# Optimization experiments

Hardware: AMD Instinct MI355X
Metric: run time of the kernel (lower is better)

## Reference

```python
import jax, jax.numpy as jnp
import numpy as np
import math

ANSWER_LEN = 11; D_MODEL = 6; FFN_DIM = 3; HEAD_DIM = 3; MAX_SEQ_LEN = 34
N_HEADS = 2; POS_DIM = 3; TOK_DIM = 3; VOCAB_SIZE = 14; MAX_DIGITS = 10
EOS_TOKEN = 12; EQUALS_TOKEN = 11; PAD_TOKEN = 13; PLUS_TOKEN = 10
B, T = 65536, 34


def _spiral(i, period):
    return (math.cos(2 * math.pi * i / period), math.sin(2 * math.pi * i / period), i / max(period - 1, 1))


def _build_pos_enc():
    N_POS = 10
    pe = np.zeros((MAX_SEQ_LEN, POS_DIM), dtype=np.float32)
    for i in range(MAX_DIGITS):
        pe[i] = _spiral(i, N_POS)
    for i in range(MAX_DIGITS):
        pe[11 + i] = _spiral(i, N_POS)
    for i in range(min(ANSWER_LEN, N_POS)):
        pe[22 + i] = _spiral(i, N_POS)
    pe[32] = [0.0, 0.0, 1.5]
    pe[10] = [2.0, 0.0, -1.0]
    pe[21] = [0.0, 2.0, -1.0]
    pe[33] = [-2.0, 0.0, -1.0]
    return pe


def _build_tok_emb():
    emb = np.zeros((VOCAB_SIZE, TOK_DIM), dtype=np.float32)
    for d in range(10):
        emb[d] = _spiral(d, 10)
    emb[PLUS_TOKEN] = [2.0, 0.0, -1.0]
    emb[EQUALS_TOKEN] = [0.0, 2.0, -1.0]
    emb[EOS_TOKEN] = [-2.0, 0.0, -1.0]
    emb[PAD_TOKEN] = [0.0, -2.0, -1.0]
    return emb


def setup_inputs() -> dict:
    key = jax.random.key(0)
    ks = jax.random.split(key, 12)
    H = N_HEADS * HEAD_DIM  # 6

    def lin(k, out_d, in_d):
        bound = 1.0 / math.sqrt(in_d)
        return jax.random.uniform(k, (out_d, in_d), jnp.float32, -bound, bound)

    return {
        'idx': jax.random.randint(ks[0], (B, T), 0, VOCAB_SIZE),
        'tok_emb': jnp.asarray(_build_tok_emb()),
        'pos_enc': jnp.asarray(_build_pos_enc()),
        'q_w': lin(ks[1], H, POS_DIM),
        'k_w': lin(ks[2], H, POS_DIM),
        'v_w': lin(ks[3], H, TOK_DIM),
        'out_w': lin(ks[4], D_MODEL, H),
        'ln1_g': jnp.ones((D_MODEL,)), 'ln1_b': jnp.zeros((D_MODEL,)),
        'ln2_g': jnp.ones((D_MODEL,)), 'ln2_b': jnp.zeros((D_MODEL,)),
        'lnf_g': jnp.ones((D_MODEL,)), 'lnf_b': jnp.zeros((D_MODEL,)),
        'ffn_w1': lin(ks[5], FFN_DIM, D_MODEL),
        'ffn_b1': jax.random.uniform(ks[6], (FFN_DIM,), jnp.float32, -1/math.sqrt(D_MODEL), 1/math.sqrt(D_MODEL)),
        'ffn_w2': lin(ks[7], D_MODEL, FFN_DIM),
        'ffn_b2': jax.random.uniform(ks[8], (D_MODEL,), jnp.float32, -1/math.sqrt(FFN_DIM), 1/math.sqrt(FFN_DIM)),
        'head_w': lin(ks[9], TOK_DIM, D_MODEL),
    }


def _ln(x, g, b, eps=1e-5):
    mu = jnp.mean(x, -1, keepdims=True)
    var = jnp.mean((x - mu) ** 2, -1, keepdims=True)
    return (x - mu) * jax.lax.rsqrt(var + eps) * g + b


def reference(idx, tok_emb, pos_enc, q_w, k_w, v_w, out_w,
              ln1_g, ln1_b, ln2_g, ln2_b, lnf_g, lnf_b,
              ffn_w1, ffn_b1, ffn_w2, ffn_b2, head_w):
    b, t = idx.shape
    tok = tok_emb[idx]                              # [B,T,3]
    pos = jnp.broadcast_to(pos_enc[:t][None], (b, t, POS_DIM))
    x = jnp.concatenate([tok, pos], -1)             # [B,T,6]
    h = _ln(x, ln1_g, ln1_b)
    x_tok, x_pos = h[..., :TOK_DIM], h[..., TOK_DIM:]
    q = (x_pos @ q_w.T).reshape(b, t, N_HEADS, HEAD_DIM)
    k = (x_pos @ k_w.T).reshape(b, t, N_HEADS, HEAD_DIM)
    v = (x_tok @ v_w.T).reshape(b, t, N_HEADS, HEAD_DIM)
    attn = jnp.einsum('bqhd,bkhd->bhqk', q, k) / math.sqrt(HEAD_DIM)
    mask = jnp.tril(jnp.ones((t, t), dtype=bool))
    attn = jnp.where(mask[None, None], attn, -jnp.inf)
    attn = jax.nn.softmax(attn, -1)
    out = jnp.einsum('bhqk,bkhd->bqhd', attn, v).reshape(b, t, N_HEADS * HEAD_DIM)
    x = x + out @ out_w.T
    h2 = _ln(x, ln2_g, ln2_b)
    ffn = jax.nn.gelu(h2 @ ffn_w1.T + ffn_b1, approximate=False) @ ffn_w2.T + ffn_b2
    x = x + ffn
    x = _ln(x, lnf_g, lnf_b)
    return (x @ head_w.T) @ tok_emb.T               # [B,T,VOCAB]
```

## Files before the change

### kernel.cpp

```cpp
#include <hip/hip_runtime.h>
#include <math.h>

#define TT  34
#define VV  14
#define BLK 512

typedef float v2f __attribute__((ext_vector_type(2)));
typedef float v4f __attribute__((ext_vector_type(4)));

#if __has_builtin(__builtin_amdgcn_exp2f)
#define EXP2F(x) __builtin_amdgcn_exp2f(x)
#else
#define EXP2F(x) exp2f(x)
#endif
#if __has_builtin(__builtin_amdgcn_rcpf)
#define RCPF(x) __builtin_amdgcn_rcpf(x)
#else
#define RCPF(x) (1.0f/(x))
#endif

static __device__ __forceinline__ v2f fma2(v2f a, v2f b, v2f c) {
    return __builtin_elementwise_fma(a, b, c);
}
static __device__ __forceinline__ v2f bc2(float s) { v2f r; r.x = s; r.y = s; return r; }
#define SV2(v, a, b) __builtin_shufflevector((v), (v), (a), (b))


__global__ __launch_bounds__(BLK, 8) void addtx_fwd(
    const int*   __restrict__ idx,
    const float* __restrict__ tok_emb,
    const float* __restrict__ pos_enc,
    const float* __restrict__ q_w,
    const float* __restrict__ k_w,
    const float* __restrict__ v_w,
    const float* __restrict__ out_w,
    const float* __restrict__ ln1_g, const float* __restrict__ ln1_b,
    const float* __restrict__ ln2_g, const float* __restrict__ ln2_b,
    const float* __restrict__ lnf_g, const float* __restrict__ lnf_b,
    const float* __restrict__ ffn_w1, const float* __restrict__ ffn_b1,
    const float* __restrict__ ffn_w2, const float* __restrict__ ffn_b2,
    const float* __restrict__ head_w,
    float* __restrict__ out, int n)
{
    __shared__ v4f   kvs[1792];
    __shared__ float wsm[308];
    __shared__ int   idsb[594];

    const int tid = threadIdx.x;
    const int blk = blockIdx.x;

    if (tid < 308) {
        const int i = tid;
        float val = 0.0f;
        if (i < 36)       { const int j = i / 6, d = i - j * 6; val = out_w[d * 6 + j]; }
        else if (i < 42)  val = ln2_g[i - 36];
        else if (i < 48)  val = ln2_b[i - 42];
        else if (i < 60)  { const int k = i - 48, d = k >> 1, ii = k & 1; val = ffn_w1[ii * 6 + d]; }
        else if (i < 66)  val = ffn_w1[12 + (i - 60)];
        else if (i < 69)  val = ffn_b1[i - 66];
        else if (i < 70)  val = 0.0f;
        else if (i < 88)  { const int k = i - 70, ii = k / 6, d = k - ii * 6; val = ffn_w2[d * 3 + ii]; }
        else if (i < 94)  val = ffn_b2[i - 88];
        else if (i < 96)  val = 0.0f;
        else if (i < 108) { const int k = i - 96, d = k >> 1, c = k & 1; val = lnf_g[d] * head_w[c * 6 + d]; }
        else if (i < 114) { const int d = i - 108; val = lnf_g[d] * head_w[12 + d]; }
        else if (i < 118) val = 0.0f;
        else if (i < 121) { const int c = i - 118; float s = 0.0f;
                            #pragma unroll
                            for (int d = 0; d < 6; ++d) s += lnf_b[d] * head_w[c * 6 + d];
                            val = s; }
        else if (i < 122) val = 0.0f;
        else if (i < 164) { const int k = i - 122, c = k / 14, v = k - c * 14; val = tok_emb[v * 3 + c]; }
        else if (i < 206) val = tok_emb[i - 164];
        else              val = pos_enc[i - 206];
        wsm[i] = val;
    }

    const int p0 = blk * BLK;
    const int b0 = p0 / TT;
    {
        const int gb = b0 * TT;
        for (int e = tid; e < 594; e += BLK) {
            const int g = gb + e;
            idsb[e] = (g < n) ? (idx[g] * 48) : 0;
        }
    }

    const float rs3l = 0.57735026918962576f * 1.4426950408889634f;
    for (int e = tid; e < TT * VV; e += BLK) {
        const int pos = e / VV, id = e - pos * VV;
        float x[6];
        x[0] = tok_emb[id * 3 + 0]; x[1] = tok_emb[id * 3 + 1]; x[2] = tok_emb[id * 3 + 2];
        x[3] = pos_enc[pos * 3 + 0]; x[4] = pos_enc[pos * 3 + 1]; x[5] = pos_enc[pos * 3 + 2];
        float mu = (x[0] + x[1] + x[2] + x[3] + x[4] + x[5]) * (1.0f / 6.0f);
        float var = 0.0f;
        #pragma unroll
        for (int d = 0; d < 6; ++d) { float dd = x[d] - mu; var += dd * dd; }
        const float rstd = rsqrtf(var * (1.0f / 6.0f) + 1e-5f);
        float h[6];
        #pragma unroll
        for (int d = 0; d < 6; ++d) h[d] = (x[d] - mu) * rstd * ln1_g[d] + ln1_b[d];
        float kk[6], vvv[6];
        #pragma unroll
        for (int r = 0; r < 6; ++r) {
            kk[r]  = (h[3] * k_w[r * 3 + 0] + h[4] * k_w[r * 3 + 1] + h[5] * k_w[r * 3 + 2]) * rs3l;
            vvv[r] =  h[0] * v_w[r * 3 + 0] + h[1] * v_w[r * 3 + 1] + h[2] * v_w[r * 3 + 2];
        }
        v4f f0; f0.x = kk[0]; f0.y = kk[3]; f0.z = kk[1]; f0.w = kk[4];
        v4f f1; f1.x = kk[2]; f1.y = kk[5]; f1.z = vvv[0]; f1.w = vvv[3];
        v4f f2; f2.x = vvv[1]; f2.y = vvv[4]; f2.z = vvv[2]; f2.w = vvv[5];
        kvs[e * 3 + 0] = f0;
        kvs[e * 3 + 1] = f1;
        kvs[e * 3 + 2] = f2;
    }
    __syncthreads();

    const int srank = (tid + ((blk & 7) << 6)) & (BLK - 1);
    const int r0 = p0 % TT;
    const int thrA = 15 * r0;
    int t, dlt, ksel;
    if (srank < thrA)           { t = srank / 15; ksel = srank - 15 * t; dlt = t - r0 + TT; }
    else if (srank < thrA + 32) { const int rr = srank - thrA; dlt = rr >> 4; ksel = rr & 15; t = r0 + dlt; }
    else                        { const int rr = srank - thrA - 32; const int qq = rr / 15;
                                  ksel = rr - 15 * qq; dlt = 2 + qq; t = r0 + dlt; }
    const int il   = dlt + TT * ksel;
    const int flat = p0 + il;
    const int b    = flat / TT;
    const int* __restrict__ rowL = idsb + (b - b0) * TT;

    float x[6];
    {
        const int tb = rowL[t] >> 4;
        x[0] = wsm[164 + tb]; x[1] = wsm[165 + tb]; x[2] = wsm[166 + tb];
        x[3] = wsm[206 + t * 3]; x[4] = wsm[207 + t * 3]; x[5] = wsm[208 + t * 3];
    }
    float q[6];
    {
        float mu = (x[0] + x[1] + x[2] + x[3] + x[4] + x[5]) * (1.0f / 6.0f);
        float var = 0.0f;
        #pragma unroll
        for (int d = 0; d < 6; ++d) { float dd = x[d] - mu; var += dd * dd; }
        const float rstd = rsqrtf(var * (1.0f / 6.0f) + 1e-5f);
        const float h3 = (x[3] - mu) * rstd * ln1_g[3] + ln1_b[3];
        const float h4 = (x[4] - mu) * rstd * ln1_g[4] + ln1_b[4];
        const float h5 = (x[5] - mu) * rstd * ln1_g[5] + ln1_b[5];
        #pragma unroll
        for (int r = 0; r < 6; ++r)
            q[r] = h3 * q_w[r * 3 + 0] + h4 * q_w[r * 3 + 1] + h5 * q_w[r * 3 + 2];
    }
    const v2f Q03 = {q[0], q[3]}, Q14 = {q[1], q[4]}, Q25 = {q[2], q[5]};

    v2f L = {0.f, 0.f}, A0 = {0.f, 0.f}, A1 = {0.f, 0.f}, A2 = {0.f, 0.f};
    int ids48 = rowL[0];
    const char* kp = (const char*)kvs;
    for (int s = 0; s <= t; ++s) {
        const v4f* e4 = (const v4f*)(kp + ids48);
        const v4f ka = e4[0], kb = e4[1], vb = e4[2];
        ids48 = rowL[s + 1];
        v2f sc = fma2(Q03, SV2(ka, 0, 1),
                 fma2(Q14, SV2(ka, 2, 3),
                      Q25 * SV2(kb, 0, 1)));
        v2f p; p.x = EXP2F(sc.x); p.y = EXP2F(sc.y);
        L += p;
        A0 = fma2(p, SV2(kb, 2, 3), A0);
        A1 = fma2(p, SV2(vb, 0, 1), A1);
        A2 = fma2(p, SV2(vb, 2, 3), A2);
        kp += VV * 48;
    }
    v2f I; I.x = RCPF(L.x); I.y = RCPF(L.y);
    const v2f O0 = A0 * I, O1 = A1 * I, O2 = A2 * I;
    const float o6[6] = {O0.x, O1.x, O2.x, O0.y, O1.y, O2.y};

    v2f X0 = {x[0], x[1]}, X1 = {x[2], x[3]}, X2 = {x[4], x[5]};
    #define LD2(i) (*reinterpret_cast<const v2f*>(&wsm[(i)]))
    #pragma unroll
    for (int j = 0; j < 6; ++j) {
        const v2f oj = bc2(o6[j]);
        X0 = fma2(oj, LD2(j * 6 + 0), X0);
        X1 = fma2(oj, LD2(j * 6 + 2), X1);
        X2 = fma2(oj, LD2(j * 6 + 4), X2);
    }

    {
        v2f S = X0 + X1 + X2;
        const float mu = (S.x + S.y) * (1.0f / 6.0f);
        const v2f muv = bc2(mu);
        const v2f D0 = X0 - muv, D1 = X1 - muv, D2 = X2 - muv;
        v2f E = fma2(D0, D0, fma2(D1, D1, D2 * D2));
        const float rstd = rsqrtf((E.x + E.y) * (1.0f / 6.0f) + 1e-5f);
        const v2f rs = bc2(rstd);
        const v2f H0 = fma2(D0 * rs, LD2(36), LD2(42));
        const v2f H1 = fma2(D1 * rs, LD2(38), LD2(44));
        const v2f H2 = fma2(D2 * rs, LD2(40), LD2(46));
        const float h[6] = {H0.x, H0.y, H1.x, H1.y, H2.x, H2.y};
        v2f F = LD2(66);
        float f2 = wsm[68];
        #pragma unroll
        for (int d = 0; d < 6; ++d) {
            F  = fma2(bc2(h[d]), LD2(48 + 2 * d), F);
            f2 = fmaf(h[d], wsm[60 + d], f2);
        }
        float g3[3];
        g3[0] = 0.5f * F.x * (1.0f + erff(F.x * 0.70710678118654752f));
        g3[1] = 0.5f * F.y * (1.0f + erff(F.y * 0.70710678118654752f));
        g3[2] = 0.5f * f2  * (1.0f + erff(f2  * 0.70710678118654752f));
        X0 += LD2(88); X1 += LD2(90); X2 += LD2(92);
        #pragma unroll
        for (int i = 0; i < 3; ++i) {
            const v2f gi = bc2(g3[i]);
            X0 = fma2(gi, LD2(70 + i * 6 + 0), X0);
            X1 = fma2(gi, LD2(70 + i * 6 + 2), X1);
            X2 = fma2(gi, LD2(70 + i * 6 + 4), X2);
        }
    }

    v2f lgv[7];
    {
        v2f S = X0 + X1 + X2;
        const float mu = (S.x + S.y) * (1.0f / 6.0f);
        const v2f muv = bc2(mu);
        const v2f D0 = X0 - muv, D1 = X1 - muv, D2 = X2 - muv;
        v2f E = fma2(D0, D0, fma2(D1, D1, D2 * D2));
        const float rstd = rsqrtf((E.x + E.y) * (1.0f / 6.0f) + 1e-5f);
        const float xd[6] = {D0.x, D0.y, D1.x, D1.y, D2.x, D2.y};
        v2f D01 = {0.f, 0.f};
        float d2 = 0.f;
        #pragma unroll
        for (int d = 0; d < 6; ++d) {
            D01 = fma2(bc2(xd[d]), LD2(96 + 2 * d), D01);
            d2  = fmaf(xd[d], wsm[108 + d], d2);
        }
        const v2f y01 = fma2(bc2(rstd), D01, LD2(118));
        const float y2 = fmaf(rstd, d2, wsm[120]);
        const v2f Y0 = bc2(y01.x), Y1 = bc2(y01.y), Y2 = bc2(y2);
        #pragma unroll
        for (int mm = 0; mm < 7; ++mm)
            lgv[mm] = fma2(Y0, LD2(122 + 2 * mm),
                      fma2(Y1, LD2(136 + 2 * mm),
                           Y2 * LD2(150 + 2 * mm)));
    }
    __syncthreads();

    v2f* lg2 = reinterpret_cast<v2f*>(kvs);
    #pragma unroll
    for (int j = 0; j < 7; ++j)
        lg2[il * 7 + j] = lgv[j];
    __syncthreads();
    const v2f* s2 = reinterpret_cast<const v2f*>(kvs);
    v2f* __restrict__ ob2 = reinterpret_cast<v2f*>(out + (size_t)blk * (BLK * VV));
    #pragma unroll
    for (int j = 0; j < 7; ++j)
        ob2[j * BLK + tid] = s2[j * BLK + tid];
}

extern "C" void kernel_launch(void* const* d_in, const int* in_sizes, int n_in,
                              void* d_out, int out_size, void* d_ws, size_t ws_size,
                              hipStream_t stream) {
    const int*   idx     = (const int*)  d_in[0];
    const float* tok_emb = (const float*)d_in[1];
    const float* pos_enc = (const float*)d_in[2];
    const float* q_w     = (const float*)d_in[3];
    const float* k_w     = (const float*)d_in[4];
    const float* v_w     = (const float*)d_in[5];
    const float* out_w   = (const float*)d_in[6];
    const float* ln1_g   = (const float*)d_in[7];
    const float* ln1_b   = (const float*)d_in[8];
    const float* ln2_g   = (const float*)d_in[9];
    const float* ln2_b   = (const float*)d_in[10];
    const float* lnf_g   = (const float*)d_in[11];
    const float* lnf_b   = (const float*)d_in[12];
    const float* ffn_w1  = (const float*)d_in[13];
    const float* ffn_b1  = (const float*)d_in[14];
    const float* ffn_w2  = (const float*)d_in[15];
    const float* ffn_b2  = (const float*)d_in[16];
    const float* head_w  = (const float*)d_in[17];
    float* out = (float*)d_out;

    const int n = in_sizes[0];
    const int blocks = n / BLK;
    addtx_fwd<<<blocks, BLK, 0, stream>>>(idx, tok_emb, pos_enc, q_w, k_w, v_w, out_w,
                                          ln1_g, ln1_b, ln2_g, ln2_b, lnf_g, lnf_b,
                                          ffn_w1, ffn_b1, ffn_w2, ffn_b2, head_w, out, n);
}
```

Baseline: 212.2 us.

## Remap work so each wave handles one position across 64 sequences

Work is reorganized so each block covers 64 sequences and a band of query positions (five blocks per chunk: positions 0-1, 2-9, 10-17, 18-25, 26-33). Each wave handles one position across 64 sequences, which removes the staggered load-balancing map and gives uniform loop trip counts within a wave. Token ids are stored transposed as 16-bit values. The LDS staging of output logits is replaced by direct per-thread vectorized global stores. The change also lowers launch_bounds occupancy to 4, computes K/V tables only for rows up to the block's band, and leaves 6 of 8 waves idle in the position-0/1 block. The direct stores are strided by 56 bytes across lanes, so they coalesce worse than the previous staged writes.

```diff
diff --git a/kernel.cpp b/kernel.cpp
--- a/kernel.cpp
+++ b/kernel.cpp
@@ -24,9 +24,10 @@
 }
 static __device__ __forceinline__ v2f bc2(float s) { v2f r; r.x = s; r.y = s; return r; }
 #define SV2(v, a, b) __builtin_shufflevector((v), (v), (a), (b))
-
-
-__global__ __launch_bounds__(BLK, 8) void addtx_fwd(
+#define LD2(i) (*reinterpret_cast<const v2f*>(&wsm[(i)]))
+
+
+__global__ __launch_bounds__(BLK, 4) void addtx_fwd(
     const int*   __restrict__ idx,
     const float* __restrict__ tok_emb,
     const float* __restrict__ pos_enc,
@@ -40,14 +41,20 @@
     const float* __restrict__ ffn_w1, const float* __restrict__ ffn_b1,
     const float* __restrict__ ffn_w2, const float* __restrict__ ffn_b2,
     const float* __restrict__ head_w,
-    float* __restrict__ out, int n)
+    float* __restrict__ out)
 {
-    __shared__ v4f   kvs[1792];
-    __shared__ float wsm[308];
-    __shared__ int   idsb[594];
+    __shared__ v4f            kvs[TT * VV * 3];
+    __shared__ float          wsm[308];
+    __shared__ unsigned short ids16[35 * 64];
 
     const int tid = threadIdx.x;
-    const int blk = blockIdx.x;
+    const int bid = blockIdx.x;
+    const int c   = bid % 5;
+    const int sc  = bid / 5;
+    const int b0  = sc * 64;
+    const int t_base = (c == 4) ? 0 : (2 + 8 * c);
+    const int nt     = (c == 4) ? 2 : 8;
+    const int nrow   = t_base + nt;
 
     if (tid < 308) {
         const int i = tid;
@@ -62,32 +69,32 @@
         else if (i < 88)  { const int k = i - 70, ii = k / 6, d = k - ii * 6; val = ffn_w2[d * 3 + ii]; }
         else if (i < 94)  val = ffn_b2[i - 88];
         else if (i < 96)  val = 0.0f;
-        else if (i < 108) { const int k = i - 96, d = k >> 1, c = k & 1; val = lnf_g[d] * head_w[c * 6 + d]; }
+        else if (i < 108) { const int k = i - 96, d = k >> 1, cc = k & 1; val = lnf_g[d] * head_w[cc * 6 + d]; }
         else if (i < 114) { const int d = i - 108; val = lnf_g[d] * head_w[12 + d]; }
         else if (i < 118) val = 0.0f;
-        else if (i < 121) { const int c = i - 118; float s = 0.0f;
+        else if (i < 121) { const int cc = i - 118; float s = 0.0f;
                             #pragma unroll
-                            for (int d = 0; d < 6; ++d) s += lnf_b[d] * head_w[c * 6 + d];
+                            for (int d = 0; d < 6; ++d) s += lnf_b[d] * head_w[cc * 6 + d];
                             val = s; }
         else if (i < 122) val = 0.0f;
-        else if (i < 164) { const int k = i - 122, c = k / 14, v = k - c * 14; val = tok_emb[v * 3 + c]; }
+        else if (i < 164) { const int k = i - 122, cc = k / 14, v = k - cc * 14; val = tok_emb[v * 3 + cc]; }
         else if (i < 206) val = tok_emb[i - 164];
         else              val = pos_enc[i - 206];
         wsm[i] = val;
     }
 
-    const int p0 = blk * BLK;
-    const int b0 = p0 / TT;
     {
         const int gb = b0 * TT;
-        for (int e = tid; e < 594; e += BLK) {
-            const int g = gb + e;
-            idsb[e] = (g < n) ? (idx[g] * 48) : 0;
-        }
+        for (int e = tid; e < 64 * TT; e += BLK) {
+            const int v  = idx[gb + e];
+            const int bl = e / TT, s = e - bl * TT;
+            ids16[s * 64 + bl] = (unsigned short)(v * 48);
+        }
+        if (tid < 64) ids16[TT * 64 + tid] = 0;
     }
 
     const float rs3l = 0.57735026918962576f * 1.4426950408889634f;
-    for (int e = tid; e < TT * VV; e += BLK) {
+    for (int e = tid; e < nrow * VV; e += BLK) {
         const int pos = e / VV, id = e - pos * VV;
         float x[6];
         x[0] = tok_emb[id * 3 + 0]; x[1] = tok_emb[id * 3 + 1]; x[2] = tok_emb[id * 3 + 2];
@@ -115,25 +122,16 @@
     }
     __syncthreads();
 
-    const int srank = (tid + ((blk & 7) << 6)) & (BLK - 1);
-    const int r0 = p0 % TT;
-    const int thrA = 15 * r0;
-    int t, dlt, ksel;
-    if (srank < thrA)           { t = srank / 15; ksel = srank - 15 * t; dlt = t - r0 + TT; }
-    else if (srank < thrA + 32) { const int rr = srank - thrA; dlt = rr >> 4; ksel = rr & 15; t = r0 + dlt; }
-    else                        { const int rr = srank - thrA - 32; const int qq = rr / 15;
-                                  ksel = rr - 15 * qq; dlt = 2 + qq; t = r0 + dlt; }
-    const int il   = dlt + TT * ksel;
-    const int flat = p0 + il;
-    const int b    = flat / TT;
-    const int* __restrict__ rowL = idsb + (b - b0) * TT;
+    const int w = tid >> 6, lane = tid & 63;
+    const int t = t_base + w;
+    if (w >= nt) return;
+    const int b = b0 + lane;
 
     float x[6];
-    {
-        const int tb = rowL[t] >> 4;
-        x[0] = wsm[164 + tb]; x[1] = wsm[165 + tb]; x[2] = wsm[166 + tb];
-        x[3] = wsm[206 + t * 3]; x[4] = wsm[207 + t * 3]; x[5] = wsm[208 + t * 3];
-    }
+    const int tb3 = ((int)ids16[t * 64 + lane]) >> 4;
+    x[0] = wsm[164 + tb3]; x[1] = wsm[165 + tb3]; x[2] = wsm[166 + tb3];
+    x[3] = wsm[206 + t * 3]; x[4] = wsm[207 + t * 3]; x[5] = wsm[208 + t * 3];
+
     float q[6];
     {
         float mu = (x[0] + x[1] + x[2] + x[3] + x[4] + x[5]) * (1.0f / 6.0f);
@@ -151,12 +149,12 @@
     const v2f Q03 = {q[0], q[3]}, Q14 = {q[1], q[4]}, Q25 = {q[2], q[5]};
 
     v2f L = {0.f, 0.f}, A0 = {0.f, 0.f}, A1 = {0.f, 0.f}, A2 = {0.f, 0.f};
-    int ids48 = rowL[0];
+    int ids48 = (int)ids16[lane];
     const char* kp = (const char*)kvs;
     for (int s = 0; s <= t; ++s) {
         const v4f* e4 = (const v4f*)(kp + ids48);
         const v4f ka = e4[0], kb = e4[1], vb = e4[2];
-        ids48 = rowL[s + 1];
+        ids48 = (int)ids16[(s + 1) * 64 + lane];
         v2f sc = fma2(Q03, SV2(ka, 0, 1),
                  fma2(Q14, SV2(ka, 2, 3),
                       Q25 * SV2(kb, 0, 1)));
@@ -172,7 +170,6 @@
     const float o6[6] = {O0.x, O1.x, O2.x, O0.y, O1.y, O2.y};
 
     v2f X0 = {x[0], x[1]}, X1 = {x[2], x[3]}, X2 = {x[4], x[5]};
-    #define LD2(i) (*reinterpret_cast<const v2f*>(&wsm[(i)]))
     #pragma unroll
     for (int j = 0; j < 6; ++j) {
         const v2f oj = bc2(o6[j]);
@@ -239,18 +236,26 @@
                       fma2(Y1, LD2(136 + 2 * mm),
                            Y2 * LD2(150 + 2 * mm)));
     }
-    __syncthreads();
-
-    v2f* lg2 = reinterpret_cast<v2f*>(kvs);
-    #pragma unroll
-    for (int j = 0; j < 7; ++j)
-        lg2[il * 7 + j] = lgv[j];
-    __syncthreads();
-    const v2f* s2 = reinterpret_cast<const v2f*>(kvs);
-    v2f* __restrict__ ob2 = reinterpret_cast<v2f*>(out + (size_t)blk * (BLK * VV));
-    #pragma unroll
-    for (int j = 0; j < 7; ++j)
-        ob2[j * BLK + tid] = s2[j * BLK + tid];
+
+    const int eidx = b * TT + t;
+    float* __restrict__ outp = out + (size_t)eidx * VV;
+    if (!(eidx & 1)) {
+        v4f w0; w0.x = lgv[0].x; w0.y = lgv[0].y; w0.z = lgv[1].x; w0.w = lgv[1].y;
+        v4f w1; w1.x = lgv[2].x; w1.y = lgv[2].y; w1.z = lgv[3].x; w1.w = lgv[3].y;
+        v4f w2; w2.x = lgv[4].x; w2.y = lgv[4].y; w2.z = lgv[5].x; w2.w = lgv[5].y;
+        *reinterpret_cast<v4f*>(outp + 0) = w0;
+        *reinterpret_cast<v4f*>(outp + 4) = w1;
+        *reinterpret_cast<v4f*>(outp + 8) = w2;
+        *reinterpret_cast<v2f*>(outp + 12) = lgv[6];
+    } else {
+        *reinterpret_cast<v2f*>(outp + 0) = lgv[0];
+        v4f w0; w0.x = lgv[1].x; w0.y = lgv[1].y; w0.z = lgv[2].x; w0.w = lgv[2].y;
+        v4f w1; w1.x = lgv[3].x; w1.y = lgv[3].y; w1.z = lgv[4].x; w1.w = lgv[4].y;
+        v4f w2; w2.x = lgv[5].x; w2.y = lgv[5].y; w2.z = lgv[6].x; w2.w = lgv[6].y;
+        *reinterpret_cast<v4f*>(outp + 2)  = w0;
+        *reinterpret_cast<v4f*>(outp + 6)  = w1;
+        *reinterpret_cast<v4f*>(outp + 10) = w2;
+    }
 }
 
 extern "C" void kernel_launch(void* const* d_in, const int* in_sizes, int n_in,
@@ -276,9 +281,11 @@
     const float* head_w  = (const float*)d_in[17];
     float* out = (float*)d_out;
 
-    const int n = in_sizes[0];
-    const int blocks = n / BLK;
+    const int n      = in_sizes[0];
+    const int seqs   = n / TT;
+    const int chunks = seqs / 64;
+    const int blocks = chunks * 5;
     addtx_fwd<<<blocks, BLK, 0, stream>>>(idx, tok_emb, pos_enc, q_w, k_w, v_w, out_w,
                                           ln1_g, ln1_b, ln2_g, ln2_b, lnf_g, lnf_b,
-                                          ffn_w1, ffn_b1, ffn_w2, ffn_b2, head_w, out, n);
+                                          ffn_w1, ffn_b1, ffn_w2, ffn_b2, head_w, out);
 }
```

After: 242.6 us. +14.4%, slower.

## Unroll attention loop by two and write logits directly without LDS staging

Applied to the files above, without the earlier changes.

The causal attention loop is unrolled by two, so two key/value entries are loaded from LDS before their exp and accumulate steps run, which exposes more independent work. The output epilogue no longer stages logits through shared memory behind two barriers. Each thread now writes its 14 logits straight to global memory with 16-byte and 8-byte stores, aligned according to row parity. LDS shrinks to exactly the KV table, and the launch-bounds occupancy hint drops from 8 to 4 blocks, which gives the compiler more registers but the direct stores are less coalesced across the wavefront.

```diff
diff --git a/kernel.cpp b/kernel.cpp
--- a/kernel.cpp
+++ b/kernel.cpp
@@ -24,9 +24,10 @@
 }
 static __device__ __forceinline__ v2f bc2(float s) { v2f r; r.x = s; r.y = s; return r; }
 #define SV2(v, a, b) __builtin_shufflevector((v), (v), (a), (b))
-
-
-__global__ __launch_bounds__(BLK, 8) void addtx_fwd(
+#define LD2(i) (*reinterpret_cast<const v2f*>(&wsm[(i)]))
+
+
+__global__ __launch_bounds__(BLK, 4) void addtx_fwd(
     const int*   __restrict__ idx,
     const float* __restrict__ tok_emb,
     const float* __restrict__ pos_enc,
@@ -42,7 +43,7 @@
     const float* __restrict__ head_w,
     float* __restrict__ out, int n)
 {
-    __shared__ v4f   kvs[1792];
+    __shared__ v4f   kvs[TT * VV * 3];
     __shared__ float wsm[308];
     __shared__ int   idsb[594];
 
@@ -151,28 +152,40 @@
     const v2f Q03 = {q[0], q[3]}, Q14 = {q[1], q[4]}, Q25 = {q[2], q[5]};
 
     v2f L = {0.f, 0.f}, A0 = {0.f, 0.f}, A1 = {0.f, 0.f}, A2 = {0.f, 0.f};
-    int ids48 = rowL[0];
     const char* kp = (const char*)kvs;
-    for (int s = 0; s <= t; ++s) {
-        const v4f* e4 = (const v4f*)(kp + ids48);
-        const v4f ka = e4[0], kb = e4[1], vb = e4[2];
-        ids48 = rowL[s + 1];
-        v2f sc = fma2(Q03, SV2(ka, 0, 1),
-                 fma2(Q14, SV2(ka, 2, 3),
-                      Q25 * SV2(kb, 0, 1)));
-        v2f p; p.x = EXP2F(sc.x); p.y = EXP2F(sc.y);
-        L += p;
-        A0 = fma2(p, SV2(kb, 2, 3), A0);
-        A1 = fma2(p, SV2(vb, 0, 1), A1);
-        A2 = fma2(p, SV2(vb, 2, 3), A2);
-        kp += VV * 48;
+    int ids_a = rowL[0];
+    int s = 0;
+    for (; s + 1 <= t; s += 2) {
+        const int ids_b = rowL[s + 1];
+        const v4f* ea = (const v4f*)(kp + ids_a);
+        const v4f* eb = (const v4f*)(kp + (VV * 48) + ids_b);
+        const v4f ka0 = ea[0], kb0 = ea[1], vb0 = ea[2];
+        const v4f ka1 = eb[0], kb1 = eb[1], vb1 = eb[2];
+        ids_a = rowL[s + 2];
+        v2f sc0 = fma2(Q03, SV2(ka0, 0, 1), fma2(Q14, SV2(ka0, 2, 3), Q25 * SV2(kb0, 0, 1)));
+        v2f sc1 = fma2(Q03, SV2(ka1, 0, 1), fma2(Q14, SV2(ka1, 2, 3), Q25 * SV2(kb1, 0, 1)));
+        v2f pp0; pp0.x = EXP2F(sc0.x); pp0.y = EXP2F(sc0.y);
+        v2f pp1; pp1.x = EXP2F(sc1.x); pp1.y = EXP2F(sc1.y);
+        L += pp0; L += pp1;
+        A0 = fma2(pp0, SV2(kb0, 2, 3), A0); A1 = fma2(pp0, SV2(vb0, 0, 1), A1); A2 = fma2(pp0, SV2(vb0, 2, 3), A2);
+        A0 = fma2(pp1, SV2(kb1, 2, 3), A0); A1 = fma2(pp1, SV2(vb1, 0, 1), A1); A2 = fma2(pp1, SV2(vb1, 2, 3), A2);
+        kp += 2 * VV * 48;
+    }
+    if (s <= t) {
+        const v4f* ea = (const v4f*)(kp + ids_a);
+        const v4f ka = ea[0], kb = ea[1], vb = ea[2];
+        v2f sc = fma2(Q03, SV2(ka, 0, 1), fma2(Q14, SV2(ka, 2, 3), Q25 * SV2(kb, 0, 1)));
+        v2f pp; pp.x = EXP2F(sc.x); pp.y = EXP2F(sc.y);
+        L += pp;
+        A0 = fma2(pp, SV2(kb, 2, 3), A0);
+        A1 = fma2(pp, SV2(vb, 0, 1), A1);
+        A2 = fma2(pp, SV2(vb, 2, 3), A2);
     }
     v2f I; I.x = RCPF(L.x); I.y = RCPF(L.y);
     const v2f O0 = A0 * I, O1 = A1 * I, O2 = A2 * I;
     const float o6[6] = {O0.x, O1.x, O2.x, O0.y, O1.y, O2.y};
 
     v2f X0 = {x[0], x[1]}, X1 = {x[2], x[3]}, X2 = {x[4], x[5]};
-    #define LD2(i) (*reinterpret_cast<const v2f*>(&wsm[(i)]))
     #pragma unroll
     for (int j = 0; j < 6; ++j) {
         const v2f oj = bc2(o6[j]);
@@ -239,18 +252,25 @@
                       fma2(Y1, LD2(136 + 2 * mm),
                            Y2 * LD2(150 + 2 * mm)));
     }
-    __syncthreads();
-
-    v2f* lg2 = reinterpret_cast<v2f*>(kvs);
-    #pragma unroll
-    for (int j = 0; j < 7; ++j)
-        lg2[il * 7 + j] = lgv[j];
-    __syncthreads();
-    const v2f* s2 = reinterpret_cast<const v2f*>(kvs);
-    v2f* __restrict__ ob2 = reinterpret_cast<v2f*>(out + (size_t)blk * (BLK * VV));
-    #pragma unroll
-    for (int j = 0; j < 7; ++j)
-        ob2[j * BLK + tid] = s2[j * BLK + tid];
+
+    float* __restrict__ outp = out + (size_t)flat * VV;
+    if (!(flat & 1)) {
+        v4f w0; w0.x = lgv[0].x; w0.y = lgv[0].y; w0.z = lgv[1].x; w0.w = lgv[1].y;
+        v4f w1; w1.x = lgv[2].x; w1.y = lgv[2].y; w1.z = lgv[3].x; w1.w = lgv[3].y;
+        v4f w2; w2.x = lgv[4].x; w2.y = lgv[4].y; w2.z = lgv[5].x; w2.w = lgv[5].y;
+        *reinterpret_cast<v4f*>(outp + 0) = w0;
+        *reinterpret_cast<v4f*>(outp + 4) = w1;
+        *reinterpret_cast<v4f*>(outp + 8) = w2;
+        *reinterpret_cast<v2f*>(outp + 12) = lgv[6];
+    } else {
+        *reinterpret_cast<v2f*>(outp + 0) = lgv[0];
+        v4f w0; w0.x = lgv[1].x; w0.y = lgv[1].y; w0.z = lgv[2].x; w0.w = lgv[2].y;
+        v4f w1; w1.x = lgv[3].x; w1.y = lgv[3].y; w1.z = lgv[4].x; w1.w = lgv[4].y;
+        v4f w2; w2.x = lgv[5].x; w2.y = lgv[5].y; w2.z = lgv[6].x; w2.w = lgv[6].y;
+        *reinterpret_cast<v4f*>(outp + 2)  = w0;
+        *reinterpret_cast<v4f*>(outp + 6)  = w1;
+        *reinterpret_cast<v4f*>(outp + 10) = w2;
+    }
 }
 
 extern "C" void kernel_launch(void* const* d_in, const int* in_sizes, int n_in,
```

After: 216.3 us. Within noise of the previous version (+2.0%).
